# Kernel optimization log

Measured on AMD Instinct MI355X. Metric: run time of the kernel, lower is better.

The kernel has to match this reference:

```python
import jax, jax.numpy as jnp
import numpy as np

B, T, D = 256, 256, 96   # batch, seq (== block_size), d_model
H, E = 6, 16             # n_head, d_head = d_model // n_head
DFF = 4 * D              # feedforward hidden = 384
NOISE_STD = 0.1
EPS = 1e-5               # torch LayerNorm default eps


def setup_inputs() -> dict:
    key = jax.random.key(0)
    ks = jax.random.split(key, 10)
    s = 0.02
    return {
        "x":     jax.random.normal(ks[0], (B, T, D), jnp.float32),
        # per-head Q/K/V projections stacked: [H, D, E] (no bias, as in Head)
        "Wq":    jax.random.normal(ks[1], (H, D, E), jnp.float32) * s,
        "Wk":    jax.random.normal(ks[2], (H, D, E), jnp.float32) * s,
        "Wv":    jax.random.normal(ks[3], (H, D, E), jnp.float32) * s,
        "Wp":    jax.random.normal(ks[4], (D, D), jnp.float32) * s,
        "bp":    jnp.zeros((D,), jnp.float32),
        "ln1_g": jnp.ones((D,), jnp.float32),
        "ln1_b": jnp.zeros((D,), jnp.float32),
        "ln2_g": jnp.ones((D,), jnp.float32),
        "ln2_b": jnp.zeros((D,), jnp.float32),
        "W1":    jax.random.normal(ks[5], (D, DFF), jnp.float32) * s,
        "b1":    jnp.zeros((DFF,), jnp.float32),
        "W2":    jax.random.normal(ks[6], (DFF, D), jnp.float32) * s,
        "b2":    jnp.zeros((D,), jnp.float32),
    }


def layernorm(x, g, b):
    m = jnp.mean(x, axis=-1, keepdims=True)
    v = jnp.var(x, axis=-1, keepdims=True)
    return (x - m) * jax.lax.rsqrt(v + EPS) * g + b


def reference(x, Wq, Wk, Wv, Wp, bp, ln1_g, ln1_b, ln2_g, ln2_b, W1, b1, W2, b2):
    Bx, Tx, Dx = x.shape
    nk1, nk2 = jax.random.split(jax.random.key(42), 2)

    # --- self-attention branch (pre-norm) ---
    h = layernorm(x, ln1_g, ln1_b)
    q = jnp.einsum('btd,hde->bhte', h, Wq)
    k = jnp.einsum('btd,hde->bhte', h, Wk)
    v = jnp.einsum('btd,hde->bhte', h, Wv)
    scores = jnp.einsum('bhte,bhse->bhts', q, k) * (E ** -0.5)
    causal = jnp.tril(jnp.ones((Tx, Tx), bool))
    scores = jnp.where(causal, scores, -jnp.inf)
    a = jax.nn.softmax(scores, axis=-1)      # dropout = identity (eval)
    o = jnp.einsum('bhts,bhse->bhte', a, v)
    o = o.transpose(0, 2, 1, 3).reshape(Bx, Tx, Dx)  # concat heads
    o = o @ Wp + bp
    x = x + o + jax.random.normal(nk1, x.shape, x.dtype) * NOISE_STD

    # --- feedforward branch (pre-norm) ---
    h = layernorm(x, ln2_g, ln2_b)
    f = jax.nn.relu(h @ W1 + b1) @ W2 + b2   # dropout = identity (eval)
    x = x + f + jax.random.normal(nk2, x.shape, x.dtype) * NOISE_STD
    return x
```

## Files before the change

### kernel.cpp

```cpp
#include <hip/hip_runtime.h>
#include <hip/hip_bf16.h>
#include <stdint.h>


#define B_    256
#define T_    256
#define D_    96
#define H_    6
#define E_    16
#define DFF_  384
#define BT_   (B_*T_)
#define NTOK_ (BT_*D_)
#define WPN_  (96*96)
#define W1N_  (96*384)
#define W2N_  (384*96)
#define WTOT_ (WPN_+W1N_+W2N_)

typedef __hip_bfloat16 bf16;
typedef __attribute__((ext_vector_type(8))) short v8s;
typedef __attribute__((ext_vector_type(4))) float v4f;

__device__ __forceinline__ void wfence(){ __asm__ volatile("" ::: "memory"); }

__host__ __device__ inline uint32_t rotl32(uint32_t x, int r){ return (x<<r)|(x>>(32-r)); }

__host__ __device__ inline void tf2x32(uint32_t k0, uint32_t k1, uint32_t& x0, uint32_t& x1){
  uint32_t ks2 = k0 ^ k1 ^ 0x1BD11BDAu;
  x0 += k0; x1 += k1;
#define TF_R(r) { x0 += x1; x1 = rotl32(x1, r); x1 ^= x0; }
  TF_R(13) TF_R(15) TF_R(26) TF_R(6)
  x0 += k1;  x1 += ks2 + 1u;
  TF_R(17) TF_R(29) TF_R(16) TF_R(24)
  x0 += ks2; x1 += k0 + 2u;
  TF_R(13) TF_R(15) TF_R(26) TF_R(6)
  x0 += k0;  x1 += k1 + 3u;
  TF_R(17) TF_R(29) TF_R(16) TF_R(24)
  x0 += k1;  x1 += ks2 + 4u;
  TF_R(13) TF_R(15) TF_R(26) TF_R(6)
  x0 += ks2; x1 += k0 + 5u;
#undef TF_R
}

__device__ __forceinline__ float erfinv32(float x){
  float w = -0.69314718056f * __log2f((1.0f - x) * (1.0f + x));
  float p;
  if (w < 5.0f) {
    w -= 2.5f;
    p = 2.81022636e-08f;
    p = fmaf(p, w, 3.43273939e-07f);
    p = fmaf(p, w, -3.5233877e-06f);
    p = fmaf(p, w, -4.39150654e-06f);
    p = fmaf(p, w, 0.00021858087f);
    p = fmaf(p, w, -0.00125372503f);
    p = fmaf(p, w, -0.00417768164f);
    p = fmaf(p, w, 0.246640727f);
    p = fmaf(p, w, 1.50140941f);
  } else {
    w = sqrtf(w) - 3.0f;
    p = -0.000200214257f;
    p = fmaf(p, w, 0.000100950558f);
    p = fmaf(p, w, 0.00134934322f);
    p = fmaf(p, w, -0.00367342844f);
    p = fmaf(p, w, 0.00573950773f);
    p = fmaf(p, w, -0.0076224613f);
    p = fmaf(p, w, 0.00943887047f);
    p = fmaf(p, w, 1.00167406f);
    p = fmaf(p, w, 2.83297682f);
  }
  return p * x;
}

__device__ __forceinline__ float jax_normal(uint32_t k0, uint32_t k1, uint32_t j){
  uint32_t x0 = 0u, x1 = j;
  tf2x32(k0, k1, x0, x1);
  uint32_t bits = x0 ^ x1;
  float f = __uint_as_float((bits >> 9) | 0x3F800000u) - 1.0f;
  const float lo = -0.99999994f;
  float u = fmaxf(lo, fmaf(f, 2.0f, lo));
  return 1.41421356f * erfinv32(u);
}

__device__ __forceinline__ float blo(uint32_t u){ return __uint_as_float(u << 16); }
__device__ __forceinline__ float bhi(uint32_t u){ return __uint_as_float(u & 0xFFFF0000u); }
__device__ __forceinline__ uint16_t f2b(float f){
  union { bf16 h; uint16_t u; } x; x.h = __float2bfloat16(f); return x.u;
}
__device__ __forceinline__ uint32_t packbf(float a, float b){
  return (uint32_t)f2b(a) | ((uint32_t)f2b(b) << 16);
}

__global__ __launch_bounds__(256, 3)
void k_attn_fused(const float* __restrict__ x,
                  const float* __restrict__ Wq, const float* __restrict__ Wk,
                  const float* __restrict__ Wv,
                  const float* __restrict__ g1, const float* __restrict__ bln1,
                  bf16* __restrict__ o_ws,
                  const float* __restrict__ Wp, const float* __restrict__ W1,
                  const float* __restrict__ W2, bf16* __restrict__ wbuf)
{
  __shared__ __align__(16) uint16_t hts[64*104];
  __shared__ __align__(16) uint32_t wpl[48][52];
  __shared__ __align__(16) uint16_t Ks[256][24];
  __shared__ __align__(16) uint16_t Vt[16][264];

  const int tid  = threadIdx.x;
  const int bh   = blockIdx.x;
  const int b    = bh / H_, h = bh % H_;
  const int w    = tid >> 6;
  const int lane = tid & 63;
  const int quad = lane >> 4;
  const int l15  = lane & 15;

  if (tid < 54) {
    int id = bh*54 + tid;
    const float* src; bf16* dst; int k, n, N;
    if (id < WPN_)             { src = Wp; dst = wbuf;               k = id/96; n = id%96; N = 96; }
    else if (id < WPN_ + W1N_) { int t = id - WPN_;
                                 src = W1; dst = wbuf + WPN_;        k = t/384; n = t%384; N = 384; }
    else                       { int t = id - WPN_ - W1N_;
                                 src = W2; dst = wbuf + WPN_ + W1N_; k = t/96;  n = t%96;  N = 96; }
    int idx = ((k>>3)*(N>>4) + (n>>4))*128 + ((n&15)<<3) + (k&7);
    dst[idx] = __float2bfloat16(src[(size_t)k*N + n]);
  }

  for (int idx = tid; idx < 48*48; idx += 256) {
    int c = idx / 48, dp = idx % 48;
    int mat = c >> 4, e = c & 15;
    const float* Wm = (mat == 0 ? Wk : (mat == 1 ? Wv : Wq)) + h*(D_*E_);
    wpl[c][dp] = packbf(Wm[(2*dp)*16 + e], Wm[(2*dp+1)*16 + e]);
  }

  v4f qacc[4];
  {
    const int r  = lane >> 2;
    const int cg = lane & 3;
    float gv[24], bv[24];
    #pragma unroll
    for (int i = 0; i < 24; ++i) { gv[i] = g1[cg*24 + i]; bv[i] = bln1[cg*24 + i]; }

    for (int rt = 0; rt < 4; ++rt) {
      __syncthreads();
      const int lrow = w*16 + r;
      const int row  = rt*64 + lrow;
      const float4* xp = (const float4*)(x + ((size_t)(b*256 + row)*96 + cg*24));
      float xv[24];
      #pragma unroll
      for (int p = 0; p < 6; ++p) {
        float4 t4 = xp[p];
        xv[4*p+0] = t4.x; xv[4*p+1] = t4.y; xv[4*p+2] = t4.z; xv[4*p+3] = t4.w;
      }
      float s1 = 0.f, s2 = 0.f;
      #pragma unroll
      for (int i = 0; i < 24; ++i) { s1 += xv[i]; s2 = fmaf(xv[i], xv[i], s2); }
      s1 += __shfl_xor(s1, 1); s2 += __shfl_xor(s2, 1);
      s1 += __shfl_xor(s1, 2); s2 += __shfl_xor(s2, 2);
      float mm = s1 * (1.0f/96.0f);
      float rs = rsqrtf(s2 * (1.0f/96.0f) - mm*mm + 1e-5f);
      #pragma unroll
      for (int p = 0; p < 12; ++p) {
        float h0 = (xv[2*p]   - mm)*rs*gv[2*p]   + bv[2*p];
        float h1 = (xv[2*p+1] - mm)*rs*gv[2*p+1] + bv[2*p+1];
        *(uint32_t*)&hts[lrow*104 + cg*24 + 2*p] = packbf(h0, h1);
      }
      __syncthreads();

      v8s ah[3];
      #pragma unroll
      for (int ks = 0; ks < 3; ++ks)
        ah[ks] = *(const v8s*)&hts[(w*16 + l15)*104 + ks*32 + quad*8];
      #pragma unroll
      for (int nt = 0; nt < 3; ++nt) {
        v4f acc = {0.f,0.f,0.f,0.f};
        #pragma unroll
        for (int ks = 0; ks < 3; ++ks) {
          v8s bb = *(const v8s*)&wpl[nt*16 + l15][ks*16 + quad*4];
          acc = __builtin_amdgcn_mfma_f32_16x16x32_bf16(ah[ks], bb, acc, 0, 0, 0);
        }
        int tr0 = rt*64 + w*16 + quad*4;
        if (nt == 0) {
          #pragma unroll
          for (int r2 = 0; r2 < 4; ++r2) Ks[tr0 + r2][l15] = f2b(acc[r2]);
        } else if (nt == 1) {
          *(uint32_t*)&Vt[l15][tr0]     = packbf(acc[0], acc[1]);
          *(uint32_t*)&Vt[l15][tr0 + 2] = packbf(acc[2], acc[3]);
        } else {
          qacc[rt] = acc;
        }
      }
    }
  }
  __syncthreads();

  uint16_t* Pb = &hts[(w*16)*104];
  v8s qf[4];
  v8s zero8;
  #pragma unroll
  for (int j = 0; j < 8; ++j) zero8[j] = 0;
  #pragma unroll
  for (int rt = 0; rt < 4; ++rt) {
    wfence();
    #pragma unroll
    for (int r2 = 0; r2 < 4; ++r2)
      Pb[(quad*4 + r2)*40 + l15] = f2b(qacc[rt][r2] * 0.25f);
    wfence();
    qf[rt] = (quad < 2) ? *(const v8s*)&Pb[l15*40 + quad*8] : zero8;
  }

  v8s ones;
  #pragma unroll
  for (int j = 0; j < 8; ++j) ones[j] = (short)0x3F80;

  v4f oacc[4], lac[4];
  #pragma unroll
  for (int i = 0; i < 4; ++i) { oacc[i] = (v4f){0.f,0.f,0.f,0.f}; lac[i] = (v4f){0.f,0.f,0.f,0.f}; }

  for (int sb = 0; sb < 8; ++sb) {
    v8s kf0 = (quad < 2) ? *(const v8s*)&Ks[sb*32      + l15][quad*8] : zero8;
    v8s kf1 = (quad < 2) ? *(const v8s*)&Ks[sb*32 + 16 + l15][quad*8] : zero8;
    v8s vf  = *(const v8s*)&Vt[l15][sb*32 + quad*8];
    #pragma unroll
    for (int i = 0; i < 4; ++i) {
      int mt = 4*i + w;
      if (mt >= 2*sb) {
        v4f z = {0.f,0.f,0.f,0.f};
        v4f s0 = __builtin_amdgcn_mfma_f32_16x16x32_bf16(qf[i], kf0, z, 0, 0, 0);
        v4f s1 = __builtin_amdgcn_mfma_f32_16x16x32_bf16(qf[i], kf1, z, 0, 0, 0);
        const int qb  = mt*16 + quad*4;
        const int sc0 = sb*32 + l15, sc1 = sc0 + 16;
        wfence();
        #pragma unroll
        for (int r2 = 0; r2 < 4; ++r2) {
          float p0 = (sc0 > qb + r2) ? 0.f : __expf(s0[r2]);
          float p1 = (sc1 > qb + r2) ? 0.f : __expf(s1[r2]);
          Pb[(quad*4 + r2)*40 + l15]      = f2b(p0);
          Pb[(quad*4 + r2)*40 + 16 + l15] = f2b(p1);
        }
        wfence();
        v8s pf = *(const v8s*)&Pb[l15*40 + quad*8];
        oacc[i] = __builtin_amdgcn_mfma_f32_16x16x32_bf16(pf, vf,   oacc[i], 0, 0, 0);
        lac[i]  = __builtin_amdgcn_mfma_f32_16x16x32_bf16(pf, ones, lac[i],  0, 0, 0);
      }
    }
  }

  #pragma unroll
  for (int i = 0; i < 4; ++i) {
    int mt = 4*i + w;
    #pragma unroll
    for (int r2 = 0; r2 < 4; ++r2) {
      float inv = 1.0f / lac[i][r2];
      size_t idx = ((size_t)b*256 + mt*16 + quad*4 + r2)*96 + h*16 + l15;
      o_ws[idx] = __float2bfloat16(oacc[i][r2] * inv);
    }
  }
}

__global__ __launch_bounds__(256, 4)
void k_proj_ff(const float* __restrict__ x, const bf16* __restrict__ o_ws,
               const bf16* __restrict__ wb,
               const float* __restrict__ bp,
               const float* __restrict__ g2, const float* __restrict__ bln2,
               const float* __restrict__ b1, const float* __restrict__ b2,
               float* __restrict__ out,
               uint32_t n1k0, uint32_t n1k1, uint32_t n2k0, uint32_t n2k1)
{
  __shared__ __align__(16) uint16_t x1t[64][104];
  __shared__ __align__(16) uint16_t t2 [64][104];

  const bf16* wpb = wb;
  const bf16* w1b = wb + WPN_;
  const bf16* w2b = wb + WPN_ + W1N_;

  const int tid  = threadIdx.x;
  const int w    = tid >> 6;
  const int lane = tid & 63;
  const int quad = lane >> 4;
  const int l15  = lane & 15;
  const int rowbase = blockIdx.x * 64;
  const uint32_t jbase = (uint32_t)rowbase * 96u;

  #define BFRAG(Wb, Ndiv16, nt, k8) \
    (*(const v8s*)((Wb) + (((k8)*(Ndiv16) + (nt))*128 + l15*8)))

  {
    v8s ao[3];
    #pragma unroll
    for (int ks = 0; ks < 3; ++ks)
      ao[ks] = *(const v8s*)(o_ws + (size_t)(rowbase + w*16 + l15)*96 + ks*32 + quad*8);
    #pragma unroll
    for (int nt = 0; nt < 6; ++nt) {
      int col = nt*16 + l15;
      v4f acc = {0.f,0.f,0.f,0.f};
      #pragma unroll
      for (int ks = 0; ks < 3; ++ks)
        acc = __builtin_amdgcn_mfma_f32_16x16x32_bf16(ao[ks], BFRAG(wpb, 6, nt, ks*4+quad), acc, 0, 0, 0);
      float bpv = bp[col];
      #pragma unroll
      for (int r = 0; r < 4; ++r) {
        int row = w*16 + quad*4 + r;
        uint32_t j = jbase + (uint32_t)row*96u + (uint32_t)col;
        x1t[row][col] = f2b(acc[r] + bpv + x[j] + 0.1f * jax_normal(n1k0, n1k1, j));
      }
    }
  }
  wfence();

  {
    int row = w*16 + (lane >> 2), cg = lane & 3;
    const uint32_t* xr = (const uint32_t*)&x1t[row][cg*24];
    float v[24];
    #pragma unroll
    for (int p = 0; p < 12; ++p) { uint32_t u = xr[p]; v[2*p] = blo(u); v[2*p+1] = bhi(u); }
    float s1 = 0.f, s2 = 0.f;
    #pragma unroll
    for (int i = 0; i < 24; ++i) { s1 += v[i]; s2 = fmaf(v[i], v[i], s2); }
    s1 += __shfl_xor(s1, 1); s2 += __shfl_xor(s2, 1);
    s1 += __shfl_xor(s1, 2); s2 += __shfl_xor(s2, 2);
    float mm = s1 * (1.0f/96.0f);
    float rs = rsqrtf(s2 * (1.0f/96.0f) - mm*mm + 1e-5f);
    uint32_t* hw = (uint32_t*)&t2[row][cg*24];
    #pragma unroll
    for (int p = 0; p < 12; ++p) {
      int c = cg*24 + 2*p;
      float h0 = (v[2*p]   - mm)*rs*g2[c]   + bln2[c];
      float h1 = (v[2*p+1] - mm)*rs*g2[c+1] + bln2[c+1];
      hw[p] = packbf(h0, h1);
    }
  }
  wfence();

  v8s ah[3];
  #pragma unroll
  for (int ks = 0; ks < 3; ++ks)
    ah[ks] = *(const v8s*)&t2[w*16 + l15][ks*32 + quad*8];
  v4f acc2[6];
  #pragma unroll
  for (int nt = 0; nt < 6; ++nt) acc2[nt] = (v4f){0.f,0.f,0.f,0.f};

  for (int c = 0; c < 4; ++c) {
    wfence();
    #pragma unroll
    for (int nt = 0; nt < 6; ++nt) {
      v4f a = {0.f,0.f,0.f,0.f};
      #pragma unroll
      for (int ks = 0; ks < 3; ++ks)
        a = __builtin_amdgcn_mfma_f32_16x16x32_bf16(ah[ks], BFRAG(w1b, 24, c*6+nt, ks*4+quad), a, 0, 0, 0);
      float b1v = b1[c*96 + nt*16 + l15];
      #pragma unroll
      for (int r = 0; r < 4; ++r)
        t2[w*16 + quad*4 + r][nt*16 + l15] = f2b(fmaxf(a[r] + b1v, 0.f));
    }
    wfence();
    v8s af[3];
    #pragma unroll
    for (int ks = 0; ks < 3; ++ks)
      af[ks] = *(const v8s*)&t2[w*16 + l15][ks*32 + quad*8];
    #pragma unroll
    for (int nt = 0; nt < 6; ++nt) {
      #pragma unroll
      for (int ks = 0; ks < 3; ++ks)
        acc2[nt] = __builtin_amdgcn_mfma_f32_16x16x32_bf16(af[ks], BFRAG(w2b, 6, nt, (c*3+ks)*4+quad), acc2[nt], 0, 0, 0);
    }
  }
  wfence();

  #pragma unroll
  for (int nt = 0; nt < 6; ++nt) {
    int col = nt*16 + l15;
    float b2v = b2[col];
    #pragma unroll
    for (int r = 0; r < 4; ++r) {
      int row = w*16 + quad*4 + r;
      uint32_t j = jbase + (uint32_t)row*96u + (uint32_t)col;
      float x1v = blo((uint32_t)x1t[row][col]);
      out[(size_t)rowbase*96 + (size_t)row*96 + col] =
          x1v + acc2[nt][r] + b2v + 0.1f * jax_normal(n2k0, n2k1, j);
    }
  }
  #undef BFRAG
}

__global__ __launch_bounds__(256)
void k_zero(float* __restrict__ out)
{
  int i = blockIdx.x*256 + threadIdx.x;
  if (i < NTOK_) out[i] = 0.0f;
}

extern "C" void kernel_launch(void* const* d_in, const int* in_sizes, int n_in,
                              void* d_out, int out_size, void* d_ws, size_t ws_size,
                              hipStream_t stream) {
  const float* x    = (const float*)d_in[0];
  const float* Wq   = (const float*)d_in[1];
  const float* Wk   = (const float*)d_in[2];
  const float* Wv   = (const float*)d_in[3];
  const float* Wp   = (const float*)d_in[4];
  const float* bp   = (const float*)d_in[5];
  const float* g1   = (const float*)d_in[6];
  const float* bln1 = (const float*)d_in[7];
  const float* g2   = (const float*)d_in[8];
  const float* bln2 = (const float*)d_in[9];
  const float* W1   = (const float*)d_in[10];
  const float* b1   = (const float*)d_in[11];
  const float* W2   = (const float*)d_in[12];
  const float* b2   = (const float*)d_in[13];
  float* out = (float*)d_out;

  size_t need = (size_t)NTOK_*sizeof(bf16) + (size_t)WTOT_*sizeof(bf16);
  if (ws_size < need) {
    hipLaunchKernelGGL(k_zero, dim3((NTOK_ + 255)/256), dim3(256), 0, stream, out);
    return;
  }
  bf16* o_ws = (bf16*)d_ws;
  bf16* wbuf = o_ws + NTOK_;

  uint32_t n1k0 = 0u, n1k1 = 0u; tf2x32(0u, 42u, n1k0, n1k1);
  uint32_t n2k0 = 0u, n2k1 = 1u; tf2x32(0u, 42u, n2k0, n2k1);

  hipLaunchKernelGGL(k_attn_fused, dim3(B_*H_), dim3(256), 0, stream,
                     x, Wq, Wk, Wv, g1, bln1, o_ws, Wp, W1, W2, wbuf);
  hipLaunchKernelGGL(k_proj_ff, dim3(BT_/64), dim3(256), 0, stream,
                     x, o_ws, wbuf, bp, g2, bln2, b1, b2, out,
                     n1k0, n1k1, n2k0, n2k1);
}
```

Measured before the change: 209.3 us.

## Double-buffer FFN hidden tile and interleave noise generation with MFMA work

The FF1/FF2 chunk loop in the projection+FFN kernel now uses a double-buffered LDS tile for the hidden activations. This lets FF1 for chunk c+1 be issued alongside FF2 for chunk c with fewer fences between them. The second-residual Gaussian noise is now generated in pieces between the MFMA chunks, and the bf16 residual x1 is kept in registers instead of being read back from LDS. Together these aim to overlap ALU-heavy RNG with matrix work and cut LDS traffic, at the cost of more registers and LDS that may lower occupancy.

```diff
diff --git a/kernel.cpp b/kernel.cpp
--- a/kernel.cpp
+++ b/kernel.cpp
@@ -265,7 +265,7 @@
                uint32_t n1k0, uint32_t n1k1, uint32_t n2k0, uint32_t n2k1)
 {
   __shared__ __align__(16) uint16_t x1t[64][104];
-  __shared__ __align__(16) uint16_t t2 [64][104];
+  __shared__ __align__(16) uint16_t t2 [2][64][104];
 
   const bf16* wpb = wb;
   const bf16* w1b = wb + WPN_;
@@ -282,6 +282,7 @@
   #define BFRAG(Wb, Ndiv16, nt, k8) \
     (*(const v8s*)((Wb) + (((k8)*(Ndiv16) + (nt))*128 + l15*8)))
 
+  uint32_t x1p[12];
   {
     v8s ao[3];
     #pragma unroll
@@ -295,12 +296,22 @@
       for (int ks = 0; ks < 3; ++ks)
         acc = __builtin_amdgcn_mfma_f32_16x16x32_bf16(ao[ks], BFRAG(wpb, 6, nt, ks*4+quad), acc, 0, 0, 0);
       float bpv = bp[col];
+      float f[4];
       #pragma unroll
       for (int r = 0; r < 4; ++r) {
         int row = w*16 + quad*4 + r;
         uint32_t j = jbase + (uint32_t)row*96u + (uint32_t)col;
-        x1t[row][col] = f2b(acc[r] + bpv + x[j] + 0.1f * jax_normal(n1k0, n1k1, j));
+        f[r] = acc[r] + bpv + x[j] + 0.1f * jax_normal(n1k0, n1k1, j);
       }
+      uint32_t p01 = packbf(f[0], f[1]);
+      uint32_t p23 = packbf(f[2], f[3]);
+      x1p[nt*2]   = p01;
+      x1p[nt*2+1] = p23;
+      int rb = w*16 + quad*4;
+      x1t[rb+0][col] = (uint16_t)p01;
+      x1t[rb+1][col] = (uint16_t)(p01 >> 16);
+      x1t[rb+2][col] = (uint16_t)p23;
+      x1t[rb+3][col] = (uint16_t)(p23 >> 16);
     }
   }
   wfence();
@@ -318,7 +329,7 @@
     s1 += __shfl_xor(s1, 2); s2 += __shfl_xor(s2, 2);
     float mm = s1 * (1.0f/96.0f);
     float rs = rsqrtf(s2 * (1.0f/96.0f) - mm*mm + 1e-5f);
-    uint32_t* hw = (uint32_t*)&t2[row][cg*24];
+    uint32_t* hw = (uint32_t*)&t2[0][row][cg*24];
     #pragma unroll
     for (int p = 0; p < 12; ++p) {
       int c = cg*24 + 2*p;
@@ -332,37 +343,62 @@
   v8s ah[3];
   #pragma unroll
   for (int ks = 0; ks < 3; ++ks)
-    ah[ks] = *(const v8s*)&t2[w*16 + l15][ks*32 + quad*8];
+    ah[ks] = *(const v8s*)&t2[0][w*16 + l15][ks*32 + quad*8];
   v4f acc2[6];
   #pragma unroll
   for (int nt = 0; nt < 6; ++nt) acc2[nt] = (v4f){0.f,0.f,0.f,0.f};
-
-  for (int c = 0; c < 4; ++c) {
-    wfence();
-    #pragma unroll
-    for (int nt = 0; nt < 6; ++nt) {
-      v4f a = {0.f,0.f,0.f,0.f};
-      #pragma unroll
-      for (int ks = 0; ks < 3; ++ks)
-        a = __builtin_amdgcn_mfma_f32_16x16x32_bf16(ah[ks], BFRAG(w1b, 24, c*6+nt, ks*4+quad), a, 0, 0, 0);
-      float b1v = b1[c*96 + nt*16 + l15];
-      #pragma unroll
-      for (int r = 0; r < 4; ++r)
-        t2[w*16 + quad*4 + r][nt*16 + l15] = f2b(fmaxf(a[r] + b1v, 0.f));
-    }
-    wfence();
-    v8s af[3];
-    #pragma unroll
-    for (int ks = 0; ks < 3; ++ks)
-      af[ks] = *(const v8s*)&t2[w*16 + l15][ks*32 + quad*8];
-    #pragma unroll
-    for (int nt = 0; nt < 6; ++nt) {
-      #pragma unroll
-      for (int ks = 0; ks < 3; ++ks)
-        acc2[nt] = __builtin_amdgcn_mfma_f32_16x16x32_bf16(af[ks], BFRAG(w2b, 6, nt, (c*3+ks)*4+quad), acc2[nt], 0, 0, 0);
-    }
-  }
-  wfence();
+  float n2v[24];
+
+  #define FF1C(C, DST) { \
+    _Pragma("unroll") \
+    for (int nt = 0; nt < 6; ++nt) { \
+      v4f a = {0.f,0.f,0.f,0.f}; \
+      _Pragma("unroll") \
+      for (int ks = 0; ks < 3; ++ks) \
+        a = __builtin_amdgcn_mfma_f32_16x16x32_bf16(ah[ks], BFRAG(w1b, 24, (C)*6+nt, ks*4+quad), a, 0, 0, 0); \
+      float b1v = b1[(C)*96 + nt*16 + l15]; \
+      _Pragma("unroll") \
+      for (int r = 0; r < 4; ++r) \
+        DST[w*16 + quad*4 + r][nt*16 + l15] = f2b(fmaxf(a[r] + b1v, 0.f)); \
+    } }
+
+  #define FF2C(C, SRC) { \
+    v8s af[3]; \
+    _Pragma("unroll") \
+    for (int ks = 0; ks < 3; ++ks) \
+      af[ks] = *(const v8s*)&SRC[w*16 + l15][ks*32 + quad*8]; \
+    _Pragma("unroll") \
+    for (int nt = 0; nt < 6; ++nt) { \
+      _Pragma("unroll") \
+      for (int ks = 0; ks < 3; ++ks) \
+        acc2[nt] = __builtin_amdgcn_mfma_f32_16x16x32_bf16(af[ks], BFRAG(w2b, 6, nt, ((C)*3+ks)*4+quad), acc2[nt], 0, 0, 0); \
+    } }
+
+  #define GEN6(C) { \
+    _Pragma("unroll") \
+    for (int i = 0; i < 6; ++i) { \
+      int vv = (C)*6 + i; int nt2 = vv >> 2; int r2 = vv & 3; \
+      int row = w*16 + quad*4 + r2; \
+      uint32_t j = jbase + (uint32_t)row*96u + (uint32_t)(nt2*16 + l15); \
+      n2v[vv] = jax_normal(n2k0, n2k1, j); \
+    } }
+
+  FF1C(0, t2[1])
+  wfence();
+  FF1C(1, t2[0])
+  FF2C(0, t2[1])
+  GEN6(0)
+  wfence();
+  FF1C(2, t2[1])
+  FF2C(1, t2[0])
+  GEN6(1)
+  wfence();
+  FF1C(3, t2[0])
+  FF2C(2, t2[1])
+  GEN6(2)
+  wfence();
+  FF2C(3, t2[0])
+  GEN6(3)
 
   #pragma unroll
   for (int nt = 0; nt < 6; ++nt) {
@@ -371,12 +407,15 @@
     #pragma unroll
     for (int r = 0; r < 4; ++r) {
       int row = w*16 + quad*4 + r;
-      uint32_t j = jbase + (uint32_t)row*96u + (uint32_t)col;
-      float x1v = blo((uint32_t)x1t[row][col]);
-      out[(size_t)rowbase*96 + (size_t)row*96 + col] =
-          x1v + acc2[nt][r] + b2v + 0.1f * jax_normal(n2k0, n2k1, j);
-    }
-  }
+      uint32_t pk = x1p[nt*2 + (r>>1)];
+      float x1v = (r&1) ? bhi(pk) : blo(pk);
+      out[(size_t)(rowbase + row)*96 + col] =
+          x1v + acc2[nt][r] + b2v + 0.1f * n2v[nt*4 + r];
+    }
+  }
+  #undef GEN6
+  #undef FF2C
+  #undef FF1C
   #undef BFRAG
 }
 
```

After: 196.9 us. -5.9%, faster.

## Split k_proj_ff work across wave pairs with 32-row tiles and split-K FFN

Applied to the files above, without the earlier changes.

k_proj_ff now handles 32 rows per block, and each 16-row tile is shared by a pair of waves. In the projection and LayerNorm stages each wave of the pair owns half the output columns, and the row statistics are combined through a small shared array. In the FFN, each wave owns half the hidden chunks, and the partial second-GEMM accumulators are exchanged through LDS before the final write. The residual stays in registers instead of an LDS tile, LDS per block shrinks, and launch bounds rise to 6 blocks per CU. The intent is more parallelism per row and higher occupancy, at the cost of extra __syncthreads, more blocks, and a cross-wave reduction.

```diff
diff --git a/kernel.cpp b/kernel.cpp
--- a/kernel.cpp
+++ b/kernel.cpp
@@ -255,7 +255,7 @@
   }
 }
 
-__global__ __launch_bounds__(256, 4)
+__global__ __launch_bounds__(256, 6)
 void k_proj_ff(const float* __restrict__ x, const bf16* __restrict__ o_ws,
                const bf16* __restrict__ wb,
                const float* __restrict__ bp,
@@ -264,8 +264,9 @@
                float* __restrict__ out,
                uint32_t n1k0, uint32_t n1k1, uint32_t n2k0, uint32_t n2k1)
 {
-  __shared__ __align__(16) uint16_t x1t[64][104];
-  __shared__ __align__(16) uint16_t t2 [64][104];
+  __shared__ __align__(16) uint16_t t2h[32][104];
+  __shared__ __align__(16) uint16_t f1w[4][16][104];
+  __shared__ __align__(8)  float2  st[32][2];
 
   const bf16* wpb = wb;
   const bf16* w1b = wb + WPN_;
@@ -273,22 +274,27 @@
 
   const int tid  = threadIdx.x;
   const int w    = tid >> 6;
+  const int wp   = w >> 1;
+  const int s    = w & 1;
   const int lane = tid & 63;
   const int quad = lane >> 4;
   const int l15  = lane & 15;
-  const int rowbase = blockIdx.x * 64;
+  const int rowbase = blockIdx.x * 32;
   const uint32_t jbase = (uint32_t)rowbase * 96u;
+  const int rloc = wp*16 + quad*4;
 
   #define BFRAG(Wb, Ndiv16, nt, k8) \
     (*(const v8s*)((Wb) + (((k8)*(Ndiv16) + (nt))*128 + l15*8)))
 
+  float ff[12];
   {
     v8s ao[3];
     #pragma unroll
     for (int ks = 0; ks < 3; ++ks)
-      ao[ks] = *(const v8s*)(o_ws + (size_t)(rowbase + w*16 + l15)*96 + ks*32 + quad*8);
-    #pragma unroll
-    for (int nt = 0; nt < 6; ++nt) {
+      ao[ks] = *(const v8s*)(o_ws + (size_t)(rowbase + wp*16 + l15)*96 + ks*32 + quad*8);
+    #pragma unroll
+    for (int nt3 = 0; nt3 < 3; ++nt3) {
+      int nt = s*3 + nt3;
       int col = nt*16 + l15;
       v4f acc = {0.f,0.f,0.f,0.f};
       #pragma unroll
@@ -297,84 +303,121 @@
       float bpv = bp[col];
       #pragma unroll
       for (int r = 0; r < 4; ++r) {
-        int row = w*16 + quad*4 + r;
+        int row = rloc + r;
         uint32_t j = jbase + (uint32_t)row*96u + (uint32_t)col;
-        x1t[row][col] = f2b(acc[r] + bpv + x[j] + 0.1f * jax_normal(n1k0, n1k1, j));
+        ff[nt3*4+r] = acc[r] + bpv + x[j] + 0.1f * jax_normal(n1k0, n1k1, j);
       }
     }
   }
-  wfence();
 
   {
-    int row = w*16 + (lane >> 2), cg = lane & 3;
-    const uint32_t* xr = (const uint32_t*)&x1t[row][cg*24];
-    float v[24];
-    #pragma unroll
-    for (int p = 0; p < 12; ++p) { uint32_t u = xr[p]; v[2*p] = blo(u); v[2*p+1] = bhi(u); }
-    float s1 = 0.f, s2 = 0.f;
-    #pragma unroll
-    for (int i = 0; i < 24; ++i) { s1 += v[i]; s2 = fmaf(v[i], v[i], s2); }
-    s1 += __shfl_xor(s1, 1); s2 += __shfl_xor(s2, 1);
-    s1 += __shfl_xor(s1, 2); s2 += __shfl_xor(s2, 2);
-    float mm = s1 * (1.0f/96.0f);
-    float rs = rsqrtf(s2 * (1.0f/96.0f) - mm*mm + 1e-5f);
-    uint32_t* hw = (uint32_t*)&t2[row][cg*24];
-    #pragma unroll
-    for (int p = 0; p < 12; ++p) {
-      int c = cg*24 + 2*p;
-      float h0 = (v[2*p]   - mm)*rs*g2[c]   + bln2[c];
-      float h1 = (v[2*p+1] - mm)*rs*g2[c+1] + bln2[c+1];
-      hw[p] = packbf(h0, h1);
-    }
-  }
-  wfence();
+    float s1p[4], s2p[4];
+    #pragma unroll
+    for (int r = 0; r < 4; ++r) {
+      float s1 = 0.f, s2 = 0.f;
+      #pragma unroll
+      for (int nt3 = 0; nt3 < 3; ++nt3) { float v = ff[nt3*4+r]; s1 += v; s2 = fmaf(v, v, s2); }
+      s1 += __shfl_xor(s1, 1); s2 += __shfl_xor(s2, 1);
+      s1 += __shfl_xor(s1, 2); s2 += __shfl_xor(s2, 2);
+      s1 += __shfl_xor(s1, 4); s2 += __shfl_xor(s2, 4);
+      s1 += __shfl_xor(s1, 8); s2 += __shfl_xor(s2, 8);
+      s1p[r] = s1; s2p[r] = s2;
+    }
+    if (l15 == 0) {
+      #pragma unroll
+      for (int r = 0; r < 4; ++r) st[rloc + r][s] = make_float2(s1p[r], s2p[r]);
+    }
+    __syncthreads();
+
+    float g2v[3], b2l[3];
+    #pragma unroll
+    for (int nt3 = 0; nt3 < 3; ++nt3) {
+      g2v[nt3] = g2[s*48 + nt3*16 + l15];
+      b2l[nt3] = bln2[s*48 + nt3*16 + l15];
+    }
+    #pragma unroll
+    for (int r = 0; r < 4; ++r) {
+      float2 pa = st[rloc + r][0], pb = st[rloc + r][1];
+      float s1 = pa.x + pb.x, s2 = pa.y + pb.y;
+      float mm = s1 * (1.0f/96.0f);
+      float rs = rsqrtf(s2 * (1.0f/96.0f) - mm*mm + 1e-5f);
+      #pragma unroll
+      for (int nt3 = 0; nt3 < 3; ++nt3)
+        t2h[rloc + r][s*48 + nt3*16 + l15] =
+            f2b((ff[nt3*4+r] - mm) * rs * g2v[nt3] + b2l[nt3]);
+    }
+  }
+  __syncthreads();
+
+  uint32_t ffp[6];
+  #pragma unroll
+  for (int nt3 = 0; nt3 < 3; ++nt3) {
+    ffp[nt3*2]   = packbf(ff[nt3*4+0], ff[nt3*4+1]);
+    ffp[nt3*2+1] = packbf(ff[nt3*4+2], ff[nt3*4+3]);
+  }
 
   v8s ah[3];
   #pragma unroll
   for (int ks = 0; ks < 3; ++ks)
-    ah[ks] = *(const v8s*)&t2[w*16 + l15][ks*32 + quad*8];
+    ah[ks] = *(const v8s*)&t2h[wp*16 + l15][ks*32 + quad*8];
   v4f acc2[6];
   #pragma unroll
   for (int nt = 0; nt < 6; ++nt) acc2[nt] = (v4f){0.f,0.f,0.f,0.f};
-
-  for (int c = 0; c < 4; ++c) {
+  uint16_t (*f1)[104] = f1w[w];
+
+  #pragma unroll
+  for (int c = 0; c < 2; ++c) {
+    const int C = s*2 + c;
     wfence();
     #pragma unroll
     for (int nt = 0; nt < 6; ++nt) {
       v4f a = {0.f,0.f,0.f,0.f};
       #pragma unroll
       for (int ks = 0; ks < 3; ++ks)
-        a = __builtin_amdgcn_mfma_f32_16x16x32_bf16(ah[ks], BFRAG(w1b, 24, c*6+nt, ks*4+quad), a, 0, 0, 0);
-      float b1v = b1[c*96 + nt*16 + l15];
+        a = __builtin_amdgcn_mfma_f32_16x16x32_bf16(ah[ks], BFRAG(w1b, 24, C*6 + nt, ks*4+quad), a, 0, 0, 0);
+      float b1v = b1[C*96 + nt*16 + l15];
       #pragma unroll
       for (int r = 0; r < 4; ++r)
-        t2[w*16 + quad*4 + r][nt*16 + l15] = f2b(fmaxf(a[r] + b1v, 0.f));
+        f1[quad*4 + r][nt*16 + l15] = f2b(fmaxf(a[r] + b1v, 0.f));
     }
     wfence();
     v8s af[3];
     #pragma unroll
     for (int ks = 0; ks < 3; ++ks)
-      af[ks] = *(const v8s*)&t2[w*16 + l15][ks*32 + quad*8];
+      af[ks] = *(const v8s*)&f1[l15][ks*32 + quad*8];
     #pragma unroll
     for (int nt = 0; nt < 6; ++nt) {
       #pragma unroll
       for (int ks = 0; ks < 3; ++ks)
-        acc2[nt] = __builtin_amdgcn_mfma_f32_16x16x32_bf16(af[ks], BFRAG(w2b, 6, nt, (c*3+ks)*4+quad), acc2[nt], 0, 0, 0);
-    }
-  }
+        acc2[nt] = __builtin_amdgcn_mfma_f32_16x16x32_bf16(af[ks], BFRAG(w2b, 6, nt, (C*3+ks)*4+quad), acc2[nt], 0, 0, 0);
+    }
+  }
+
   wfence();
-
-  #pragma unroll
-  for (int nt = 0; nt < 6; ++nt) {
-    int col = nt*16 + l15;
+  {
+    float* exw = (float*)&f1w[w][0][0];
+    #pragma unroll
+    for (int nt3 = 0; nt3 < 3; ++nt3)
+      #pragma unroll
+      for (int r = 0; r < 4; ++r)
+        exw[(quad*4 + r)*49 + nt3*16 + l15] = acc2[(1-s)*3 + nt3][r];
+  }
+  __syncthreads();
+  const float* exr = (const float*)&f1w[wp*2 + (1-s)][0][0];
+
+  #pragma unroll
+  for (int nt3 = 0; nt3 < 3; ++nt3) {
+    int col = s*48 + nt3*16 + l15;
     float b2v = b2[col];
     #pragma unroll
     for (int r = 0; r < 4; ++r) {
-      int row = w*16 + quad*4 + r;
+      int row = rloc + r;
       uint32_t j = jbase + (uint32_t)row*96u + (uint32_t)col;
-      float x1v = blo((uint32_t)x1t[row][col]);
-      out[(size_t)rowbase*96 + (size_t)row*96 + col] =
-          x1v + acc2[nt][r] + b2v + 0.1f * jax_normal(n2k0, n2k1, j);
+      uint32_t pk = ffp[nt3*2 + (r>>1)];
+      float x1v = (r&1) ? bhi(pk) : blo(pk);
+      float part = exr[(quad*4 + r)*49 + nt3*16 + l15];
+      out[(size_t)(rowbase + row)*96 + col] =
+          x1v + (acc2[s*3 + nt3][r] + part) + b2v + 0.1f * jax_normal(n2k0, n2k1, j);
     }
   }
   #undef BFRAG
@@ -419,7 +462,7 @@
 
   hipLaunchKernelGGL(k_attn_fused, dim3(B_*H_), dim3(256), 0, stream,
                      x, Wq, Wk, Wv, g1, bln1, o_ws, Wp, W1, W2, wbuf);
-  hipLaunchKernelGGL(k_proj_ff, dim3(BT_/64), dim3(256), 0, stream,
+  hipLaunchKernelGGL(k_proj_ff, dim3(BT_/32), dim3(256), 0, stream,
                      x, o_ws, wbuf, bp, g2, bln2, b1, b2, out,
                      n1k0, n1k1, n2k0, n2k1);
 }
```

New measurement: 212.9 us. About the same (+1.7%).
